# Kernel optimization log

Hardware: AMD Instinct MI355X
Metric: run time of the kernel (lower is better)

The kernel has to match this reference:

```python
import jax, jax.numpy as jnp
import numpy as np

N, E, D, H1, H2 = 50000, 800000, 128, 128, 128


def setup_inputs() -> dict:
    key = jax.random.key(0)
    ks = jax.random.split(key, 9)
    s = 0.05
    return {
        "x": jax.random.normal(ks[0], (N, D), dtype=jnp.float32),
        "edge_index": jax.random.randint(ks[1], (2, E), 0, N, dtype=jnp.int64),
        "W_l1": jax.random.normal(ks[2], (D, H1), dtype=jnp.float32) * s,
        "b_l1": jnp.zeros((H1,), dtype=jnp.float32),
        "W_r1": jax.random.normal(ks[3], (D, H1), dtype=jnp.float32) * s,
        "W_l2": jax.random.normal(ks[4], (H1, H2), dtype=jnp.float32) * s,
        "b_l2": jnp.zeros((H2,), dtype=jnp.float32),
        "W_r2": jax.random.normal(ks[5], (H1, H2), dtype=jnp.float32) * s,
        "W_e": jax.random.normal(ks[6], (2 * H2, 1), dtype=jnp.float32) * s,
        "b_e": jnp.zeros((1,), dtype=jnp.float32),
    }


def _sage_conv(h, src, tgt, n_nodes, W_l, b_l, W_r):
    # PyG SAGEConv (mean aggr): out = lin_l(mean_{j in N(i)} h_j) + lin_r(h_i)
    msg = h[src]                                              # [E, F] gather
    agg = jax.ops.segment_sum(msg, tgt, num_segments=n_nodes)  # [N, F]
    cnt = jax.ops.segment_sum(jnp.ones((src.shape[0], 1), h.dtype), tgt,
                              num_segments=n_nodes)            # [N, 1]
    mean = agg / jnp.maximum(cnt, 1.0)                         # empty nbrs -> 0
    return mean @ W_l + b_l + h @ W_r


def reference(x, edge_index, W_l1, b_l1, W_r1, W_l2, b_l2, W_r2, W_e, b_e):
    src, tgt = edge_index[0], edge_index[1]
    n_nodes = x.shape[0]
    h = jax.nn.relu(_sage_conv(x, src, tgt, n_nodes, W_l1, b_l1, W_r1))
    # dropout is identity in eval mode
    h = _sage_conv(h, src, tgt, n_nodes, W_l2, b_l2, W_r2)
    z = jnp.concatenate([h[src], h[tgt]], axis=-1)  # [E, 2*H2]
    y = z @ W_e + b_e                                # [E, 1]
    return jax.nn.sigmoid(y)
```

## Files before the change

### kernel.cpp

```cpp
#include <hip/hip_runtime.h>

#define NN 50000
#define NE 800000
#define DD 128
#define BUCKETS 196
#define PB 4096
#define PBLK 196
#define EMAX 6144
#define BPAD 264
#define PACKB 6250

typedef unsigned int uint_t;
typedef unsigned short ush_t;
typedef __attribute__((ext_vector_type(8))) short short8;
typedef __attribute__((ext_vector_type(4))) float f32x4;

__device__ __forceinline__ float bflo(uint_t u) { return __uint_as_float(u << 16); }
__device__ __forceinline__ float bfhi(uint_t u) { return __uint_as_float(u & 0xffff0000u); }
__device__ __forceinline__ ush_t f2bf(float f) {
  uint_t u = __float_as_uint(f);
  u += 0x7fffu + ((u >> 16) & 1u);
  return (ush_t)(u >> 16);
}
__device__ __forceinline__ uint_t pack2(float a, float b) {
  return (uint_t)f2bf(a) | ((uint_t)f2bf(b) << 16);
}

__device__ __forceinline__ int ld_idx(const void* ei, int is64, long long i) {
  return is64 ? (int)((const long long*)ei)[i] : ((const int*)ei)[i];
}

__device__ __forceinline__ int detect64(const void* ei) {
  const unsigned long long* p = (const unsigned long long*)ei;
  unsigned long long w = p[threadIdx.x & 63];
  return __ballot((w >> 32) != 0) == 0ull ? 1 : 0;
}

__device__ __forceinline__ int block_incl_scan(int v, int tid, int* wsum) {
  int lane = tid & 63, wave = tid >> 6;
  int s = v;
#pragma unroll
  for (int off = 1; off < 64; off <<= 1) {
    int u = __shfl_up(s, off, 64);
    if (lane >= off) s += u;
  }
  if (lane == 63) wsum[wave] = s;
  __syncthreads();
  int base = 0;
  if (wave > 0) base += wsum[0];
  if (wave > 1) base += wsum[1];
  if (wave > 2) base += wsum[2];
  return base + s;
}

__global__ __launch_bounds__(256) void prep_part_k(
    const void* __restrict__ ei, int* __restrict__ bcur,
    uint_t* __restrict__ pbuf, uint_t* __restrict__ epk,
    const float* __restrict__ x, ush_t* __restrict__ xb,
    const float* __restrict__ Wl1, const float* __restrict__ Wr1,
    const float* __restrict__ Wl2, const float* __restrict__ Wr2,
    ush_t* __restrict__ Wt1, ush_t* __restrict__ Wt2) {
  __shared__ int hist[256];
  __shared__ int basel[256];
  __shared__ int cur[256];
  __shared__ int gbase[256];
  __shared__ int wsum[4];
  __shared__ uint_t buf[PB];
  __shared__ unsigned char bbuf[PB];
  int tid = threadIdx.x;
  int blk = blockIdx.x;
  if (blk >= PBLK) {
    blk -= PBLK;
    if (blk < PACKB) {
      int i = blk * 256 + tid;
      float4 v = reinterpret_cast<const float4*>(x)[i];
      uint2 o;
      o.x = pack2(v.x, v.y);
      o.y = pack2(v.z, v.w);
      reinterpret_cast<uint2*>(xb)[i] = o;
      return;
    }
    blk -= PACKB;
    int e = blk * 256 + tid;
    int layer = e >> 15;
    int r = e & 32767;
    int col = r >> 8;
    int k = r & 255;
    const float* Wl = layer ? Wl2 : Wl1;
    const float* Wr = layer ? Wr2 : Wr1;
    float v = (k < DD) ? Wl[k * DD + col] : Wr[(k - DD) * DD + col];
    ush_t* Wt = layer ? Wt2 : Wt1;
    Wt[col * 256 + k] = f2bf(v);
    return;
  }
  int is64 = detect64(ei);
  hist[tid] = 0;
  __syncthreads();
  long long base = (long long)blk * PB;
  uint_t pv[PB / 256];
#pragma unroll
  for (int i = 0; i < PB / 256; ++i) {
    long long e = base + i * 256 + tid;
    if (e < NE) {
      int s = ld_idx(ei, is64, e);
      int d = ld_idx(ei, is64, (long long)NE + e);
      pv[i] = ((uint_t)(d >> 8) << 24) | ((uint_t)(d & 255) << 16) | (uint_t)s;
      epk[e] = ((uint_t)d << 16) | (uint_t)s;
      atomicAdd(&hist[d >> 8], 1);
    } else {
      pv[i] = 0xFFFFFFFFu;
    }
  }
  __syncthreads();
  int hv = hist[tid];
  int incl = block_incl_scan(hv, tid, wsum);
  basel[tid] = incl - hv;
  cur[tid] = incl - hv;
  if (hv > 0) gbase[tid] = atomicAdd(&bcur[tid], hv);
  __syncthreads();
#pragma unroll
  for (int i = 0; i < PB / 256; ++i) {
    uint_t p = pv[i];
    if (p != 0xFFFFFFFFu) {
      int b = p >> 24;
      int r = atomicAdd(&cur[b], 1);
      buf[r] = p & 0xFFFFFFu;
      bbuf[r] = (unsigned char)b;
    }
  }
  __syncthreads();
  int total = basel[255] + hist[255];
  for (int j = tid; j < total; j += 256) {
    int b = bbuf[j];
    int slot = gbase[b] + (j - basel[b]);
    if (slot < EMAX) pbuf[(size_t)b * EMAX + slot] = buf[j];
  }
}

__global__ __launch_bounds__(256) void csr_k(const uint_t* __restrict__ pbuf,
                                             const int* __restrict__ bcur,
                                             int* __restrict__ offsets,
                                             int* __restrict__ srclist) {
  __shared__ int cnt[256];
  __shared__ int scur[256];
  __shared__ int wsum[4];
  __shared__ int sgb, scnt, stot;
  __shared__ uint_t ebuf[EMAX];
  int tid = threadIdx.x;
  int b = blockIdx.x;
  int v = 0;
  if (tid < BUCKETS) {
    v = bcur[tid];
    if (v > EMAX) v = EMAX;
  }
  int incl = block_incl_scan(v, tid, wsum);
  if (tid == b) { sgb = incl - v; scnt = v; }
  if (tid == BUCKETS - 1) stot = incl;
  cnt[tid] = 0;
  __syncthreads();
  int gb = sgb;
  int ecnt = scnt;
  for (int j = tid; j < ecnt; j += 256) {
    uint_t e = pbuf[(size_t)b * EMAX + j];
    ebuf[j] = e;
    atomicAdd(&cnt[(e >> 16) & 255], 1);
  }
  __syncthreads();
  int c = cnt[tid];
  int incl2 = block_incl_scan(c, tid, wsum);
  int ex = incl2 - c;
  scur[tid] = ex;
  int node = b * 256 + tid;
  if (node < NN) offsets[node] = gb + ex;
  if (b == BUCKETS - 1 && tid == 0) offsets[NN] = stot;
  __syncthreads();
  for (int j = tid; j < ecnt; j += 256) {
    uint_t e = ebuf[j];
    int p = atomicAdd(&scur[(e >> 16) & 255], 1);
    srclist[gb + p] = (int)(e & 0xFFFFu);
  }
}

__global__ __launch_bounds__(256) void agg_k(const ush_t* __restrict__ featb,
                                             const int* __restrict__ srclist,
                                             const int* __restrict__ offsets,
                                             ush_t* __restrict__ meanb) {
  int t = blockIdx.x * 256 + threadIdx.x;
  int node = t >> 4;
  int lane = t & 15;
  int f = lane << 3;
  int beg = offsets[node];
  int end = offsets[node + 1];
  float a0 = 0.f, a1 = 0.f, a2 = 0.f, a3 = 0.f, a4 = 0.f, a5 = 0.f, a6 = 0.f, a7 = 0.f;
  for (int c = beg; c < end; c += 16) {
    int idx = c + lane;
    int sl = (idx < end) ? srclist[idx] : 0;
    int m = min(16, end - c);
    int jj = 0;
    for (; jj + 4 <= m; jj += 4) {
      int s0 = __shfl(sl, jj, 16);
      int s1 = __shfl(sl, jj + 1, 16);
      int s2 = __shfl(sl, jj + 2, 16);
      int s3 = __shfl(sl, jj + 3, 16);
      uint4 v0 = *reinterpret_cast<const uint4*>(featb + (size_t)s0 * DD + f);
      uint4 v1 = *reinterpret_cast<const uint4*>(featb + (size_t)s1 * DD + f);
      uint4 v2 = *reinterpret_cast<const uint4*>(featb + (size_t)s2 * DD + f);
      uint4 v3 = *reinterpret_cast<const uint4*>(featb + (size_t)s3 * DD + f);
      a0 += bflo(v0.x); a1 += bfhi(v0.x); a2 += bflo(v0.y); a3 += bfhi(v0.y);
      a4 += bflo(v0.z); a5 += bfhi(v0.z); a6 += bflo(v0.w); a7 += bfhi(v0.w);
      a0 += bflo(v1.x); a1 += bfhi(v1.x); a2 += bflo(v1.y); a3 += bfhi(v1.y);
      a4 += bflo(v1.z); a5 += bfhi(v1.z); a6 += bflo(v1.w); a7 += bfhi(v1.w);
      a0 += bflo(v2.x); a1 += bfhi(v2.x); a2 += bflo(v2.y); a3 += bfhi(v2.y);
      a4 += bflo(v2.z); a5 += bfhi(v2.z); a6 += bflo(v2.w); a7 += bfhi(v2.w);
      a0 += bflo(v3.x); a1 += bfhi(v3.x); a2 += bflo(v3.y); a3 += bfhi(v3.y);
      a4 += bflo(v3.z); a5 += bfhi(v3.z); a6 += bflo(v3.w); a7 += bfhi(v3.w);
    }
    for (; jj < m; ++jj) {
      int s = __shfl(sl, jj, 16);
      uint4 v = *reinterpret_cast<const uint4*>(featb + (size_t)s * DD + f);
      a0 += bflo(v.x); a1 += bfhi(v.x); a2 += bflo(v.y); a3 += bfhi(v.y);
      a4 += bflo(v.z); a5 += bfhi(v.z); a6 += bflo(v.w); a7 += bfhi(v.w);
    }
  }
  float inv = 1.0f / fmaxf((float)(end - beg), 1.0f);
  uint4 o;
  o.x = pack2(a0 * inv, a1 * inv);
  o.y = pack2(a2 * inv, a3 * inv);
  o.z = pack2(a4 * inv, a5 * inv);
  o.w = pack2(a6 * inv, a7 * inv);
  *reinterpret_cast<uint4*>(meanb + (size_t)node * DD + f) = o;
}

#define MFMA_CORE(A0PTR, A1PTR, WTPTR)                                         \
  int tid = threadIdx.x;                                                       \
  int lane = tid & 63;                                                         \
  int wave = tid >> 6;                                                         \
  int n15 = lane & 15, quad = lane >> 4;                                       \
  int nb = blockIdx.x * 64;                                                    \
  for (int it = 0; it < 16; ++it) {                                            \
    int i = it * 256 + tid;                                                    \
    int col = i >> 5, c = i & 31;                                              \
    *reinterpret_cast<short8*>(&sB[col * BPAD + c * 8]) =                      \
        reinterpret_cast<const short8*>(WTPTR)[i];                             \
  }                                                                            \
  __syncthreads();                                                             \
  int row = nb + wave * 16 + n15;                                              \
  int arow = (row < NN) ? row : (NN - 1);                                      \
  const ush_t* a0 = A0PTR + (size_t)arow * DD;                                 \
  const ush_t* a1 = A1PTR + (size_t)arow * DD;                                 \
  f32x4 acc[8];                                                                \
  _Pragma("unroll")                                                            \
  for (int t = 0; t < 8; ++t) acc[t] = (f32x4){0.f, 0.f, 0.f, 0.f};           \
  _Pragma("unroll")                                                            \
  for (int c = 0; c < 8; ++c) {                                                \
    const ush_t* ap = (c < 4) ? (a0 + c * 32 + quad * 8)                       \
                              : (a1 + (c - 4) * 32 + quad * 8);                \
    short8 af = *reinterpret_cast<const short8*>(ap);                          \
    int kb = c * 32 + quad * 8;                                                \
    _Pragma("unroll")                                                          \
    for (int t = 0; t < 8; ++t) {                                              \
      short8 bf = *reinterpret_cast<const short8*>(&sB[(t * 16 + n15) * BPAD + kb]); \
      acc[t] = __builtin_amdgcn_mfma_f32_16x16x32_bf16(af, bf, acc[t], 0, 0, 0); \
    }                                                                          \
  }

__global__ __launch_bounds__(256, 2) void sage_l1(
    const ush_t* __restrict__ meanb, const ush_t* __restrict__ xb,
    const ush_t* __restrict__ Wt1, const float* __restrict__ bl,
    ush_t* __restrict__ h1b) {
  __shared__ ush_t sB[128 * BPAD];
  MFMA_CORE(meanb, xb, Wt1)
#pragma unroll
  for (int t = 0; t < 8; ++t) {
    int col = t * 16 + n15;
    float b = bl[col];
#pragma unroll
    for (int reg = 0; reg < 4; ++reg) {
      int r = nb + wave * 16 + quad * 4 + reg;
      if (r < NN)
        h1b[(size_t)r * DD + col] = f2bf(fmaxf(acc[t][reg] + b, 0.f));
    }
  }
}

__global__ __launch_bounds__(256, 2) void sage_l2(
    const ush_t* __restrict__ meanb, const ush_t* __restrict__ h1b,
    const ush_t* __restrict__ Wt2, const float* __restrict__ bl,
    const float* __restrict__ We, float2* __restrict__ s12) {
  __shared__ ush_t sB[128 * BPAD];
  MFMA_CORE(meanb, h1b, Wt2)
  float p1[4] = {0.f, 0.f, 0.f, 0.f};
  float p2[4] = {0.f, 0.f, 0.f, 0.f};
#pragma unroll
  for (int t = 0; t < 8; ++t) {
    int col = t * 16 + n15;
    float b = bl[col];
    float w1 = We[col];
    float w2 = We[DD + col];
#pragma unroll
    for (int reg = 0; reg < 4; ++reg) {
      float v = acc[t][reg] + b;
      p1[reg] += v * w1;
      p2[reg] += v * w2;
    }
  }
#pragma unroll
  for (int reg = 0; reg < 4; ++reg) {
    float v1 = p1[reg], v2 = p2[reg];
    for (int off = 8; off > 0; off >>= 1) {
      v1 += __shfl_down(v1, off, 16);
      v2 += __shfl_down(v2, off, 16);
    }
    int r = nb + wave * 16 + quad * 4 + reg;
    if (n15 == 0 && r < NN) s12[r] = make_float2(v1, v2);
  }
}

__global__ __launch_bounds__(256) void edge_k(const uint_t* __restrict__ epk,
                                              const float2* __restrict__ s12,
                                              const float* __restrict__ be,
                                              float* __restrict__ out) {
  int e = blockIdx.x * 256 + threadIdx.x;
  uint_t p = epk[e];
  float2 a = s12[p & 0xFFFFu];
  float2 b = s12[p >> 16];
  float v = a.x + b.y + be[0];
  out[e] = 1.0f / (1.0f + __expf(-v));
}

extern "C" void kernel_launch(void* const* d_in, const int* in_sizes, int n_in,
                              void* d_out, int out_size, void* d_ws, size_t ws_size,
                              hipStream_t stream) {
  const float* x   = (const float*)d_in[0];
  const void*  ei  = d_in[1];
  const float* Wl1 = (const float*)d_in[2];
  const float* bl1 = (const float*)d_in[3];
  const float* Wr1 = (const float*)d_in[4];
  const float* Wl2 = (const float*)d_in[5];
  const float* bl2 = (const float*)d_in[6];
  const float* Wr2 = (const float*)d_in[7];
  const float* We  = (const float*)d_in[8];
  const float* be  = (const float*)d_in[9];
  float* out = (float*)d_out;

  int* bcur    = (int*)d_ws;
  int* offsets = bcur + 256;
  uint_t* epk  = (uint_t*)(offsets + 50004);
  uint_t* pbuf = epk + NE;
  int* srclist = (int*)(pbuf + (size_t)BUCKETS * EMAX);
  ush_t* xb    = (ush_t*)(srclist + NE);
  ush_t* meanb = xb + (size_t)NN * DD;
  ush_t* h1b   = meanb + (size_t)NN * DD;
  float2* s12  = (float2*)(h1b + (size_t)NN * DD);
  ush_t* Wt1   = (ush_t*)((float*)s12 + 2 * NN);
  ush_t* Wt2   = Wt1 + 32768;

  hipMemsetAsync(bcur, 0, 256 * sizeof(int), stream);
  prep_part_k<<<PBLK + PACKB + 256, 256, 0, stream>>>(
      ei, bcur, pbuf, epk, x, xb, Wl1, Wr1, Wl2, Wr2, Wt1, Wt2);
  csr_k<<<BUCKETS, 256, 0, stream>>>(pbuf, bcur, offsets, srclist);

  int gemm_blocks = (NN + 63) / 64;
  agg_k<<<(NN * 16) / 256, 256, 0, stream>>>(xb, srclist, offsets, meanb);
  sage_l1<<<gemm_blocks, 256, 0, stream>>>(meanb, xb, Wt1, bl1, h1b);

  agg_k<<<(NN * 16) / 256, 256, 0, stream>>>(h1b, srclist, offsets, meanb);
  sage_l2<<<gemm_blocks, 256, 0, stream>>>(meanb, h1b, Wt2, bl2, We, s12);

  edge_k<<<NE / 256, 256, 0, stream>>>(epk, s12, be, out);
}
```

Baseline: 220.2 us.

## Fuse neighbor mean aggregation into SAGE MFMA GEMM kernels via shared memory

Each GEMM block first computes the neighbor means for its 64 rows into shared memory, then runs the MFMA matmul reading the mean operand from LDS. This removes the separate aggregation kernels and the global round-trip of the mean buffer. The weight tile is loaded in two halves to shrink LDS and allow 3 blocks per CU. The trade-off is that each block does its gather with only 16 nodes in flight per pass, which may hurt latency hiding, and the weight loading now has extra syncs.

```diff
diff --git a/kernel.cpp b/kernel.cpp
--- a/kernel.cpp
+++ b/kernel.cpp
@@ -7,8 +7,8 @@
 #define PB 4096
 #define PBLK 196
 #define EMAX 6144
-#define BPAD 264
 #define PACKB 6250
+#define MPAD 136
 
 typedef unsigned int uint_t;
 typedef unsigned short ush_t;
@@ -181,95 +181,99 @@
   }
 }
 
-__global__ __launch_bounds__(256) void agg_k(const ush_t* __restrict__ featb,
-                                             const int* __restrict__ srclist,
-                                             const int* __restrict__ offsets,
-                                             ush_t* __restrict__ meanb) {
-  int t = blockIdx.x * 256 + threadIdx.x;
-  int node = t >> 4;
-  int lane = t & 15;
-  int f = lane << 3;
-  int beg = offsets[node];
-  int end = offsets[node + 1];
-  float a0 = 0.f, a1 = 0.f, a2 = 0.f, a3 = 0.f, a4 = 0.f, a5 = 0.f, a6 = 0.f, a7 = 0.f;
-  for (int c = beg; c < end; c += 16) {
-    int idx = c + lane;
-    int sl = (idx < end) ? srclist[idx] : 0;
-    int m = min(16, end - c);
-    int jj = 0;
-    for (; jj + 4 <= m; jj += 4) {
-      int s0 = __shfl(sl, jj, 16);
-      int s1 = __shfl(sl, jj + 1, 16);
-      int s2 = __shfl(sl, jj + 2, 16);
-      int s3 = __shfl(sl, jj + 3, 16);
-      uint4 v0 = *reinterpret_cast<const uint4*>(featb + (size_t)s0 * DD + f);
-      uint4 v1 = *reinterpret_cast<const uint4*>(featb + (size_t)s1 * DD + f);
-      uint4 v2 = *reinterpret_cast<const uint4*>(featb + (size_t)s2 * DD + f);
-      uint4 v3 = *reinterpret_cast<const uint4*>(featb + (size_t)s3 * DD + f);
-      a0 += bflo(v0.x); a1 += bfhi(v0.x); a2 += bflo(v0.y); a3 += bfhi(v0.y);
-      a4 += bflo(v0.z); a5 += bfhi(v0.z); a6 += bflo(v0.w); a7 += bfhi(v0.w);
-      a0 += bflo(v1.x); a1 += bfhi(v1.x); a2 += bflo(v1.y); a3 += bfhi(v1.y);
-      a4 += bflo(v1.z); a5 += bfhi(v1.z); a6 += bflo(v1.w); a7 += bfhi(v1.w);
-      a0 += bflo(v2.x); a1 += bfhi(v2.x); a2 += bflo(v2.y); a3 += bfhi(v2.y);
-      a4 += bflo(v2.z); a5 += bfhi(v2.z); a6 += bflo(v2.w); a7 += bfhi(v2.w);
-      a0 += bflo(v3.x); a1 += bfhi(v3.x); a2 += bflo(v3.y); a3 += bfhi(v3.y);
-      a4 += bflo(v3.z); a5 += bfhi(v3.z); a6 += bflo(v3.w); a7 += bfhi(v3.w);
-    }
-    for (; jj < m; ++jj) {
-      int s = __shfl(sl, jj, 16);
-      uint4 v = *reinterpret_cast<const uint4*>(featb + (size_t)s * DD + f);
-      a0 += bflo(v.x); a1 += bfhi(v.x); a2 += bflo(v.y); a3 += bfhi(v.y);
-      a4 += bflo(v.z); a5 += bfhi(v.z); a6 += bflo(v.w); a7 += bfhi(v.w);
-    }
-  }
-  float inv = 1.0f / fmaxf((float)(end - beg), 1.0f);
-  uint4 o;
-  o.x = pack2(a0 * inv, a1 * inv);
-  o.y = pack2(a2 * inv, a3 * inv);
-  o.z = pack2(a4 * inv, a5 * inv);
-  o.w = pack2(a6 * inv, a7 * inv);
-  *reinterpret_cast<uint4*>(meanb + (size_t)node * DD + f) = o;
-}
-
-#define MFMA_CORE(A0PTR, A1PTR, WTPTR)                                         \
+#define AGG_MFMA_CORE(FEATPTR, A1PTR, WTPTR)                                   \
   int tid = threadIdx.x;                                                       \
+  int nb = blockIdx.x * 64;                                                    \
+  {                                                                            \
+    int lane16 = tid & 15;                                                     \
+    int ng = tid >> 4;                                                         \
+    int f = lane16 << 3;                                                       \
+    for (int pass = 0; pass < 4; ++pass) {                                     \
+      int ln = pass * 16 + ng;                                                 \
+      int node = nb + ln;                                                      \
+      float a0 = 0.f, a1v = 0.f, a2 = 0.f, a3 = 0.f,                           \
+            a4 = 0.f, a5 = 0.f, a6 = 0.f, a7 = 0.f;                            \
+      if (node < NN) {                                                         \
+        int beg = offsets[node], end = offsets[node + 1];                      \
+        for (int c = beg; c < end; c += 16) {                                  \
+          int idx = c + lane16;                                                \
+          int sl = (idx < end) ? srclist[idx] : 0;                             \
+          int m = min(16, end - c);                                            \
+          int jj = 0;                                                          \
+          for (; jj + 4 <= m; jj += 4) {                                       \
+            int s0 = __shfl(sl, jj, 16);                                       \
+            int s1 = __shfl(sl, jj + 1, 16);                                   \
+            int s2 = __shfl(sl, jj + 2, 16);                                   \
+            int s3 = __shfl(sl, jj + 3, 16);                                   \
+            uint4 v0 = *reinterpret_cast<const uint4*>(FEATPTR + (size_t)s0 * DD + f); \
+            uint4 v1 = *reinterpret_cast<const uint4*>(FEATPTR + (size_t)s1 * DD + f); \
+            uint4 v2 = *reinterpret_cast<const uint4*>(FEATPTR + (size_t)s2 * DD + f); \
+            uint4 v3 = *reinterpret_cast<const uint4*>(FEATPTR + (size_t)s3 * DD + f); \
+            a0 += bflo(v0.x); a1v += bfhi(v0.x); a2 += bflo(v0.y); a3 += bfhi(v0.y); \
+            a4 += bflo(v0.z); a5 += bfhi(v0.z); a6 += bflo(v0.w); a7 += bfhi(v0.w); \
+            a0 += bflo(v1.x); a1v += bfhi(v1.x); a2 += bflo(v1.y); a3 += bfhi(v1.y); \
+            a4 += bflo(v1.z); a5 += bfhi(v1.z); a6 += bflo(v1.w); a7 += bfhi(v1.w); \
+            a0 += bflo(v2.x); a1v += bfhi(v2.x); a2 += bflo(v2.y); a3 += bfhi(v2.y); \
+            a4 += bflo(v2.z); a5 += bfhi(v2.z); a6 += bflo(v2.w); a7 += bfhi(v2.w); \
+            a0 += bflo(v3.x); a1v += bfhi(v3.x); a2 += bflo(v3.y); a3 += bfhi(v3.y); \
+            a4 += bflo(v3.z); a5 += bfhi(v3.z); a6 += bflo(v3.w); a7 += bfhi(v3.w); \
+          }                                                                    \
+          for (; jj < m; ++jj) {                                               \
+            int s = __shfl(sl, jj, 16);                                        \
+            uint4 v = *reinterpret_cast<const uint4*>(FEATPTR + (size_t)s * DD + f); \
+            a0 += bflo(v.x); a1v += bfhi(v.x); a2 += bflo(v.y); a3 += bfhi(v.y); \
+            a4 += bflo(v.z); a5 += bfhi(v.z); a6 += bflo(v.w); a7 += bfhi(v.w); \
+          }                                                                    \
+        }                                                                      \
+        float inv = 1.0f / fmaxf((float)(end - beg), 1.0f);                    \
+        a0 *= inv; a1v *= inv; a2 *= inv; a3 *= inv;                           \
+        a4 *= inv; a5 *= inv; a6 *= inv; a7 *= inv;                            \
+      }                                                                        \
+      uint4 o;                                                                 \
+      o.x = pack2(a0, a1v); o.y = pack2(a2, a3);                               \
+      o.z = pack2(a4, a5);  o.w = pack2(a6, a7);                               \
+      *reinterpret_cast<uint4*>(&sM[ln * MPAD + f]) = o;                       \
+    }                                                                          \
+  }                                                                            \
   int lane = tid & 63;                                                         \
   int wave = tid >> 6;                                                         \
   int n15 = lane & 15, quad = lane >> 4;                                       \
-  int nb = blockIdx.x * 64;                                                    \
-  for (int it = 0; it < 16; ++it) {                                            \
-    int i = it * 256 + tid;                                                    \
-    int col = i >> 5, c = i & 31;                                              \
-    *reinterpret_cast<short8*>(&sB[col * BPAD + c * 8]) =                      \
-        reinterpret_cast<const short8*>(WTPTR)[i];                             \
-  }                                                                            \
-  __syncthreads();                                                             \
   int row = nb + wave * 16 + n15;                                              \
   int arow = (row < NN) ? row : (NN - 1);                                      \
-  const ush_t* a0 = A0PTR + (size_t)arow * DD;                                 \
-  const ush_t* a1 = A1PTR + (size_t)arow * DD;                                 \
+  const ush_t* a1p = A1PTR + (size_t)arow * DD;                                \
+  const ush_t* amp = &sM[(wave * 16 + n15) * MPAD];                            \
   f32x4 acc[8];                                                                \
   _Pragma("unroll")                                                            \
-  for (int t = 0; t < 8; ++t) acc[t] = (f32x4){0.f, 0.f, 0.f, 0.f};           \
-  _Pragma("unroll")                                                            \
-  for (int c = 0; c < 8; ++c) {                                                \
-    const ush_t* ap = (c < 4) ? (a0 + c * 32 + quad * 8)                       \
-                              : (a1 + (c - 4) * 32 + quad * 8);                \
-    short8 af = *reinterpret_cast<const short8*>(ap);                          \
-    int kb = c * 32 + quad * 8;                                                \
+  for (int t = 0; t < 8; ++t) acc[t] = (f32x4){0.f, 0.f, 0.f, 0.f};            \
+  for (int h = 0; h < 2; ++h) {                                                \
+    __syncthreads();                                                           \
+    for (int it = 0; it < 8; ++it) {                                           \
+      int i = it * 256 + tid;              \
+      int col = i >> 4, cc = i & 15;                                           \
+      *reinterpret_cast<short8*>(&sB[col * MPAD + cc * 8]) =                   \
+          *reinterpret_cast<const short8*>(WTPTR + col * 256 + h * 128 + cc * 8); \
+    }                                                                          \
+    __syncthreads();                                                           \
     _Pragma("unroll")                                                          \
-    for (int t = 0; t < 8; ++t) {                                              \
-      short8 bf = *reinterpret_cast<const short8*>(&sB[(t * 16 + n15) * BPAD + kb]); \
-      acc[t] = __builtin_amdgcn_mfma_f32_16x16x32_bf16(af, bf, acc[t], 0, 0, 0); \
+    for (int c = 0; c < 4; ++c) {                                              \
+      int kb = c * 32 + quad * 8;                                              \
+      short8 af = (h == 0) ? *reinterpret_cast<const short8*>(&amp[kb])        \
+                           : *reinterpret_cast<const short8*>(&a1p[kb]);       \
+      _Pragma("unroll")                                                        \
+      for (int t = 0; t < 8; ++t) {                                            \
+        short8 bf = *reinterpret_cast<const short8*>(&sB[(t * 16 + n15) * MPAD + kb]); \
+        acc[t] = __builtin_amdgcn_mfma_f32_16x16x32_bf16(af, bf, acc[t], 0, 0, 0); \
+      }                                                                        \
     }                                                                          \
   }
 
-__global__ __launch_bounds__(256, 2) void sage_l1(
-    const ush_t* __restrict__ meanb, const ush_t* __restrict__ xb,
-    const ush_t* __restrict__ Wt1, const float* __restrict__ bl,
-    ush_t* __restrict__ h1b) {
-  __shared__ ush_t sB[128 * BPAD];
-  MFMA_CORE(meanb, xb, Wt1)
+__global__ __launch_bounds__(256, 3) void agg_sage_l1(
+    const ush_t* __restrict__ xb, const int* __restrict__ srclist,
+    const int* __restrict__ offsets, const ush_t* __restrict__ Wt1,
+    const float* __restrict__ bl, ush_t* __restrict__ h1b) {
+  __shared__ __align__(16) ush_t sM[64 * MPAD];
+  __shared__ __align__(16) ush_t sB[128 * MPAD];
+  AGG_MFMA_CORE(xb, xb, Wt1)
 #pragma unroll
   for (int t = 0; t < 8; ++t) {
     int col = t * 16 + n15;
@@ -283,12 +287,14 @@
   }
 }
 
-__global__ __launch_bounds__(256, 2) void sage_l2(
-    const ush_t* __restrict__ meanb, const ush_t* __restrict__ h1b,
-    const ush_t* __restrict__ Wt2, const float* __restrict__ bl,
-    const float* __restrict__ We, float2* __restrict__ s12) {
-  __shared__ ush_t sB[128 * BPAD];
-  MFMA_CORE(meanb, h1b, Wt2)
+__global__ __launch_bounds__(256, 3) void agg_sage_l2(
+    const ush_t* __restrict__ h1b, const int* __restrict__ srclist,
+    const int* __restrict__ offsets, const ush_t* __restrict__ Wt2,
+    const float* __restrict__ bl, const float* __restrict__ We,
+    float2* __restrict__ s12) {
+  __shared__ __align__(16) ush_t sM[64 * MPAD];
+  __shared__ __align__(16) ush_t sB[128 * MPAD];
+  AGG_MFMA_CORE(h1b, h1b, Wt2)
   float p1[4] = {0.f, 0.f, 0.f, 0.f};
   float p2[4] = {0.f, 0.f, 0.f, 0.f};
 #pragma unroll
@@ -349,8 +355,7 @@
   uint_t* pbuf = epk + NE;
   int* srclist = (int*)(pbuf + (size_t)BUCKETS * EMAX);
   ush_t* xb    = (ush_t*)(srclist + NE);
-  ush_t* meanb = xb + (size_t)NN * DD;
-  ush_t* h1b   = meanb + (size_t)NN * DD;
+  ush_t* h1b   = xb + (size_t)NN * DD;
   float2* s12  = (float2*)(h1b + (size_t)NN * DD);
   ush_t* Wt1   = (ush_t*)((float*)s12 + 2 * NN);
   ush_t* Wt2   = Wt1 + 32768;
@@ -361,11 +366,8 @@
   csr_k<<<BUCKETS, 256, 0, stream>>>(pbuf, bcur, offsets, srclist);
 
   int gemm_blocks = (NN + 63) / 64;
-  agg_k<<<(NN * 16) / 256, 256, 0, stream>>>(xb, srclist, offsets, meanb);
-  sage_l1<<<gemm_blocks, 256, 0, stream>>>(meanb, xb, Wt1, bl1, h1b);
-
-  agg_k<<<(NN * 16) / 256, 256, 0, stream>>>(h1b, srclist, offsets, meanb);
-  sage_l2<<<gemm_blocks, 256, 0, stream>>>(meanb, h1b, Wt2, bl2, We, s12);
+  agg_sage_l1<<<gemm_blocks, 256, 0, stream>>>(xb, srclist, offsets, Wt1, bl1, h1b);
+  agg_sage_l2<<<gemm_blocks, 256, 0, stream>>>(h1b, srclist, offsets, Wt2, bl2, We, s12);
 
   edge_k<<<NE / 256, 256, 0, stream>>>(epk, s12, be, out);
 }
```

New measurement: 246.4 us. +11.9%, slower.

## Stream weight tile through LDS in K-quarters to raise occupancy

Applied to the files above, without the earlier changes.

The MFMA dense-layer kernels no longer stage the full 128x256 transposed weight in LDS (about 66 KB per block). They load it in four 64-wide K chunks into an 18 KB buffer, with syncs around each chunk. This cuts LDS use so launch bounds can rise from 2 to 6 blocks per CU, improving latency hiding for the row loads. The cost is extra barriers and the weights being reloaded from global/L2 per quarter with no overlap between load and compute.

```diff
diff --git a/kernel.cpp b/kernel.cpp
--- a/kernel.cpp
+++ b/kernel.cpp
@@ -7,8 +7,8 @@
 #define PB 4096
 #define PBLK 196
 #define EMAX 6144
-#define BPAD 264
 #define PACKB 6250
+#define BSTR 72
 
 typedef unsigned int uint_t;
 typedef unsigned short ush_t;
@@ -231,45 +231,45 @@
   *reinterpret_cast<uint4*>(meanb + (size_t)node * DD + f) = o;
 }
 
-#define MFMA_CORE(A0PTR, A1PTR, WTPTR)                                         \
+#define MFMA_CORE_Q(A0PTR, A1PTR, WTPTR)                                       \
   int tid = threadIdx.x;                                                       \
   int lane = tid & 63;                                                         \
   int wave = tid >> 6;                                                         \
   int n15 = lane & 15, quad = lane >> 4;                                       \
   int nb = blockIdx.x * 64;                                                    \
-  for (int it = 0; it < 16; ++it) {                                            \
-    int i = it * 256 + tid;                                                    \
-    int col = i >> 5, c = i & 31;                                              \
-    *reinterpret_cast<short8*>(&sB[col * BPAD + c * 8]) =                      \
-        reinterpret_cast<const short8*>(WTPTR)[i];                             \
-  }                                                                            \
-  __syncthreads();                                                             \
   int row = nb + wave * 16 + n15;                                              \
   int arow = (row < NN) ? row : (NN - 1);                                      \
-  const ush_t* a0 = A0PTR + (size_t)arow * DD;                                 \
-  const ush_t* a1 = A1PTR + (size_t)arow * DD;                                 \
   f32x4 acc[8];                                                                \
   _Pragma("unroll")                                                            \
-  for (int t = 0; t < 8; ++t) acc[t] = (f32x4){0.f, 0.f, 0.f, 0.f};           \
-  _Pragma("unroll")                                                            \
-  for (int c = 0; c < 8; ++c) {                                                \
-    const ush_t* ap = (c < 4) ? (a0 + c * 32 + quad * 8)                       \
-                              : (a1 + (c - 4) * 32 + quad * 8);                \
-    short8 af = *reinterpret_cast<const short8*>(ap);                          \
-    int kb = c * 32 + quad * 8;                                                \
+  for (int t = 0; t < 8; ++t) acc[t] = (f32x4){0.f, 0.f, 0.f, 0.f};            \
+  for (int q = 0; q < 4; ++q) {                                                \
+    __syncthreads();                                                           \
+    for (int i = tid; i < 1024; i += 256) {      \
+      int col = i >> 3, cc = i & 7;                                            \
+      *reinterpret_cast<short8*>(&sB[col * BSTR + cc * 8]) =                   \
+          *reinterpret_cast<const short8*>(WTPTR + col * 256 + q * 64 + cc * 8); \
+    }                                                                          \
+    __syncthreads();                                                           \
+    const ush_t* ap = (q < 2) ? (A0PTR + (size_t)arow * DD + q * 64)           \
+                              : (A1PTR + (size_t)arow * DD + (q - 2) * 64);    \
     _Pragma("unroll")                                                          \
-    for (int t = 0; t < 8; ++t) {                                              \
-      short8 bf = *reinterpret_cast<const short8*>(&sB[(t * 16 + n15) * BPAD + kb]); \
-      acc[t] = __builtin_amdgcn_mfma_f32_16x16x32_bf16(af, bf, acc[t], 0, 0, 0); \
+    for (int c2 = 0; c2 < 2; ++c2) {                                           \
+      int kl = c2 * 32 + quad * 8;                                             \
+      short8 af = *reinterpret_cast<const short8*>(ap + kl);                   \
+      _Pragma("unroll")                                                        \
+      for (int t = 0; t < 8; ++t) {                                            \
+        short8 bf = *reinterpret_cast<const short8*>(&sB[(t * 16 + n15) * BSTR + kl]); \
+        acc[t] = __builtin_amdgcn_mfma_f32_16x16x32_bf16(af, bf, acc[t], 0, 0, 0); \
+      }                                                                        \
     }                                                                          \
   }
 
-__global__ __launch_bounds__(256, 2) void sage_l1(
+__global__ __launch_bounds__(256, 6) void sage_l1(
     const ush_t* __restrict__ meanb, const ush_t* __restrict__ xb,
     const ush_t* __restrict__ Wt1, const float* __restrict__ bl,
     ush_t* __restrict__ h1b) {
-  __shared__ ush_t sB[128 * BPAD];
-  MFMA_CORE(meanb, xb, Wt1)
+  __shared__ __align__(16) ush_t sB[128 * BSTR];
+  MFMA_CORE_Q(meanb, xb, Wt1)
 #pragma unroll
   for (int t = 0; t < 8; ++t) {
     int col = t * 16 + n15;
@@ -283,12 +283,12 @@
   }
 }
 
-__global__ __launch_bounds__(256, 2) void sage_l2(
+__global__ __launch_bounds__(256, 6) void sage_l2(
     const ush_t* __restrict__ meanb, const ush_t* __restrict__ h1b,
     const ush_t* __restrict__ Wt2, const float* __restrict__ bl,
     const float* __restrict__ We, float2* __restrict__ s12) {
-  __shared__ ush_t sB[128 * BPAD];
-  MFMA_CORE(meanb, h1b, Wt2)
+  __shared__ __align__(16) ush_t sB[128 * BSTR];
+  MFMA_CORE_Q(meanb, h1b, Wt2)
   float p1[4] = {0.f, 0.f, 0.f, 0.f};
   float p2[4] = {0.f, 0.f, 0.f, 0.f};
 #pragma unroll
```

Result: no change. 222.1 us (+0.9%).
